# Optimization experiments

Measured on AMD Instinct MI355X. Metric: run time of the kernel, lower is better.

## Reference

```python
import jax, jax.numpy as jnp
import numpy as np

N_NODES = 50000
N_EDGES = 800000
IN_F = 128
OUT_F = 64


def setup_inputs() -> dict:
    key = jax.random.key(0)
    k1, k2, k3, k4, k5 = jax.random.split(key, 5)
    x = jax.random.normal(k1, (N_NODES, IN_F), dtype=jnp.float32)
    edge_index = jax.random.randint(k2, (2, N_EDGES), 0, N_NODES, dtype=jnp.int64)
    edge_weight = jax.random.uniform(k3, (N_EDGES,), dtype=jnp.float32)
    # Linear(in,out,bias=False): store as [in, out] so h = x @ W
    W = jax.random.normal(k4, (IN_F, OUT_F), dtype=jnp.float32) * (1.0 / np.sqrt(IN_F))
    # Linear(2*out, 1, bias=False): store as [2*out] vector
    a = jax.random.normal(k5, (2 * OUT_F,), dtype=jnp.float32) * (1.0 / np.sqrt(2 * OUT_F))
    return {"x": x, "edge_index": edge_index, "edge_weight": edge_weight, "W": W, "a": a}


def reference(x, edge_index, edge_weight, W, a):
    N = x.shape[0]
    F = W.shape[1]
    src, dst = edge_index[0], edge_index[1]
    h = x @ W  # [N, F]
    # a([h_src ; h_dst]) == h_src @ a[:F] + h_dst @ a[F:]  (no edge-level concat)
    s_src = h @ a[:F]   # [N]
    s_dst = h @ a[F:]   # [N]
    e = s_src[src] + s_dst[dst]            # [E]
    alpha = jax.nn.leaky_relu(e, negative_slope=0.2) * edge_weight
    alpha = alpha - jnp.max(alpha)         # global max subtraction, as in source
    alpha_exp = jnp.exp(alpha)             # [E]
    alpha_sum = jax.ops.segment_sum(alpha_exp, dst, num_segments=N)  # [N]
    alpha_norm = alpha_exp / (alpha_sum[dst] + 1e-8)                 # [E] (dropout = identity, eval mode)
    out = jax.ops.segment_sum(h[src] * alpha_norm[:, None], dst, num_segments=N)  # [N, F]
    return jax.nn.elu(out)
```

## Files before the change

kernel.cpp:

```cpp
#include <hip/hip_runtime.h>
#include <hip/hip_bf16.h>
#include <math.h>

#define FIN 128
#define FOUT 64
#define TM 64
#define XS_STRIDE 136

#define DB 64
#define CAP 1280
#define NBMAX 800
#define TILE_A 2048
#define EPT_A 8

typedef __attribute__((ext_vector_type(8))) short short8;
typedef __attribute__((ext_vector_type(4))) float floatx4;

static __device__ __forceinline__ unsigned short f2bf(float f) {
  __hip_bfloat16 b = __float2bfloat16(f);
  return *reinterpret_cast<unsigned short*>(&b);
}

__global__ __launch_bounds__(256) void k_gemm(
    const float* __restrict__ x, const float* __restrict__ W,
    const float* __restrict__ a, unsigned short* __restrict__ hbf,
    float* __restrict__ s_src, float* __restrict__ s_dst,
    int* __restrict__ bcur, int N)
{
  __shared__ unsigned short xsb[TM][XS_STRIDE];
  __shared__ unsigned short Wl[FOUT][XS_STRIDE];
  int t = threadIdx.x;
  int n0 = blockIdx.x * TM;

  int gid = blockIdx.x * 256 + t;
  if (gid < 800) bcur[gid] = 0;

  for (int i = t; i < FIN * FOUT; i += 256) {
    int k = i >> 6, f = i & 63;
    Wl[f][k] = f2bf(W[i]);
  }

#pragma unroll
  for (int i = 0; i < 8; i++) {
    int idx = t + i * 256;
    int row = idx >> 5, c4 = (idx & 31) * 4;
    int n = n0 + row;
    float4 v = make_float4(0.f, 0.f, 0.f, 0.f);
    if (n < N) v = *(const float4*)&x[(size_t)n * FIN + c4];
    ushort4 u = make_ushort4(f2bf(v.x), f2bf(v.y), f2bf(v.z), f2bf(v.w));
    *(ushort4*)&xsb[row][c4] = u;
  }
  __syncthreads();

  int lane = t & 63, w = t >> 6;
  int m = lane & 15, q = lane >> 4;

  short8 bf[4][4];
#pragma unroll
  for (int k0 = 0; k0 < 4; k0++)
#pragma unroll
    for (int j = 0; j < 4; j++)
      bf[k0][j] = *(const short8*)&Wl[j * 16 + m][k0 * 32 + q * 8];

  floatx4 acc[4];
#pragma unroll
  for (int j = 0; j < 4; j++) acc[j] = (floatx4){0.f, 0.f, 0.f, 0.f};

#pragma unroll
  for (int k0 = 0; k0 < 4; k0++) {
    short8 af = *(const short8*)&xsb[w * 16 + m][k0 * 32 + q * 8];
#pragma unroll
    for (int j = 0; j < 4; j++)
      acc[j] = __builtin_amdgcn_mfma_f32_16x16x32_bf16(af, bf[k0][j], acc[j], 0, 0, 0);
  }

  float av1[4], av2[4];
#pragma unroll
  for (int j = 0; j < 4; j++) {
    av1[j] = a[j * 16 + m];
    av2[j] = a[FOUT + j * 16 + m];
  }
  float s1r[4], s2r[4];
#pragma unroll
  for (int r = 0; r < 4; r++) {
    float c1 = 0.f, c2 = 0.f;
#pragma unroll
    for (int j = 0; j < 4; j++) {
      c1 = fmaf(acc[j][r], av1[j], c1);
      c2 = fmaf(acc[j][r], av2[j], c2);
    }
    s1r[r] = c1; s2r[r] = c2;
  }
#pragma unroll
  for (int o = 1; o < 16; o <<= 1) {
#pragma unroll
    for (int r = 0; r < 4; r++) {
      s1r[r] += __shfl_xor(s1r[r], o);
      s2r[r] += __shfl_xor(s2r[r], o);
    }
  }

#pragma unroll
  for (int j = 0; j < 4; j++)
#pragma unroll
    for (int r = 0; r < 4; r++) {
      int n = n0 + w * 16 + q * 4 + r;
      if (n < N) hbf[(size_t)n * FOUT + j * 16 + m] = f2bf(acc[j][r]);
    }
  if (m == 0) {
#pragma unroll
    for (int r = 0; r < 4; r++) {
      int n = n0 + w * 16 + q * 4 + r;
      if (n < N) { s_src[n] = s1r[r]; s_dst[n] = s2r[r]; }
    }
  }
}

__global__ __launch_bounds__(256) void k_bucketA(
    const int* __restrict__ src, const int* __restrict__ dst,
    const float* __restrict__ ew, const float* __restrict__ s_src,
    const float* __restrict__ s_dst, int* __restrict__ bcur,
    uint2* __restrict__ inter, int E, int nbuck)
{
  __shared__ uint2 stage[TILE_A];
  __shared__ int hist[NBMAX];
  __shared__ int sbase[NBMAX];
  __shared__ int gbase[NBMAX];
  __shared__ int wsum[4];

  int t = threadIdx.x;
  int base = blockIdx.x * TILE_A;
  int cntTile = E - base; if (cntTile > TILE_A) cntTile = TILE_A;

  for (int i = t; i < nbuck; i += 256) hist[i] = 0;
  __syncthreads();

  int sv[EPT_A], dv[EPT_A]; float evw[EPT_A]; int okm[EPT_A];
#pragma unroll
  for (int i = 0; i < EPT_A; i++) {
    int e = base + t + i * 256;
    okm[i] = (e < E);
    sv[i] = 0; dv[i] = 0; evw[i] = 0.f;
    if (okm[i]) { sv[i] = src[e]; dv[i] = dst[e]; evw[i] = ew[e]; }
  }

  float g1[EPT_A], g2[EPT_A];
#pragma unroll
  for (int i = 0; i < EPT_A; i++) {
    g1[i] = s_src[sv[i]];
    g2[i] = s_dst[dv[i]];
  }

  int lpos[EPT_A];
#pragma unroll
  for (int i = 0; i < EPT_A; i++)
    lpos[i] = okm[i] ? atomicAdd(&hist[dv[i] >> 6], 1) : -1;
  __syncthreads();

  int i0 = t * 4;
  int c0 = (i0 + 0 < nbuck) ? hist[i0 + 0] : 0;
  int c1 = (i0 + 1 < nbuck) ? hist[i0 + 1] : 0;
  int c2 = (i0 + 2 < nbuck) ? hist[i0 + 2] : 0;
  int c3 = (i0 + 3 < nbuck) ? hist[i0 + 3] : 0;
  int ts = c0 + c1 + c2 + c3;
  int lane = t & 63, wid = t >> 6;
  int inc = ts;
#pragma unroll
  for (int o = 1; o < 64; o <<= 1) {
    int up = __shfl_up(inc, o);
    if (lane >= o) inc += up;
  }
  if (lane == 63) wsum[wid] = inc;
  __syncthreads();
  int woff = 0;
  for (int w = 0; w < wid; w++) woff += wsum[w];
  int run = woff + inc - ts;
  if (i0 + 0 < nbuck) sbase[i0 + 0] = run; run += c0;
  if (i0 + 1 < nbuck) sbase[i0 + 1] = run; run += c1;
  if (i0 + 2 < nbuck) sbase[i0 + 2] = run; run += c2;
  if (i0 + 3 < nbuck) sbase[i0 + 3] = run;
  __syncthreads();

  for (int b = t; b < nbuck; b += 256)
    if (hist[b] > 0) gbase[b] = atomicAdd(&bcur[b], hist[b]);
  __syncthreads();

#pragma unroll
  for (int i = 0; i < EPT_A; i++) {
    if (lpos[i] >= 0) {
      float v = g1[i] + g2[i];
      v = (v > 0.f) ? v : 0.2f * v;
      v *= evw[i];
      unsigned key = ((unsigned)dv[i] << 16) | (unsigned)sv[i];
      stage[sbase[dv[i] >> 6] + lpos[i]] = make_uint2(key, __float_as_uint(__expf(v)));
    }
  }
  __syncthreads();

  for (int i = t; i < cntTile; i += 256) {
    uint2 en = stage[i];
    int b = en.x >> 22;
    int slot = gbase[b] + (i - sbase[b]);
    if (slot < CAP) inter[(size_t)b * CAP + slot] = en;
  }
}

__global__ __launch_bounds__(512) void k_bucketB(
    const uint2* __restrict__ inter, const int* __restrict__ bcur,
    const unsigned short* __restrict__ hbf, float* __restrict__ out, int N)
{
  __shared__ uint2 ss[CAP];
  __shared__ int hist[DB];
  __shared__ int rp[DB];
  int b = blockIdx.x;
  int t = threadIdx.x;
  int cnt = bcur[b]; if (cnt > CAP) cnt = CAP;

  if (t < DB) hist[t] = 0;
  __syncthreads();

  const uint2* bin = inter + (size_t)b * CAP;
  unsigned kx[3], ka[3]; int lp[3], dl[3];
#pragma unroll
  for (int i = 0; i < 3; i++) {
    int p = t + i * 512;
    lp[i] = -1;
    if (p < cnt) {
      uint2 en = bin[p];
      kx[i] = en.x; ka[i] = en.y;
      dl[i] = (en.x >> 16) & (DB - 1);
      lp[i] = atomicAdd(&hist[dl[i]], 1);
    }
  }
  __syncthreads();

  if (t < DB) {
    int v = hist[t];
    int inc = v;
#pragma unroll
    for (int o = 1; o < 64; o <<= 1) {
      int up = __shfl_up(inc, o);
      if (t >= o) inc += up;
    }
    rp[t] = inc - v;
  }
  __syncthreads();

#pragma unroll
  for (int i = 0; i < 3; i++)
    if (lp[i] >= 0) ss[rp[dl[i]] + lp[i]] = make_uint2(kx[i], ka[i]);
  __syncthreads();

  int grp = t >> 3, l = t & 7;
  int n = b * DB + grp;
  int beg = rp[grp];
  int end = beg + hist[grp];

  float acc[8];
#pragma unroll
  for (int i = 0; i < 8; i++) acc[i] = 0.f;
  float asum = 0.f;

  for (int p = beg; p < end; p += 4) {
    float aev[4]; uint4 rv[4];
#pragma unroll
    for (int u = 0; u < 4; u++) {
      aev[u] = 0.f;
      rv[u] = make_uint4(0u, 0u, 0u, 0u);
      if (p + u < end) {
        uint2 e = ss[p + u];
        aev[u] = __uint_as_float(e.y);
        rv[u] = ((const uint4*)(hbf + ((size_t)(e.x & 0xFFFFu) << 6)))[l];
      }
    }
#pragma unroll
    for (int u = 0; u < 4; u++) {
      asum += aev[u];
      const unsigned* uu = (const unsigned*)&rv[u];
#pragma unroll
      for (int i = 0; i < 4; i++) {
        float2 f = __bfloat1622float2(*(const __hip_bfloat162*)&uu[i]);
        acc[2 * i]     = fmaf(aev[u], f.x, acc[2 * i]);
        acc[2 * i + 1] = fmaf(aev[u], f.y, acc[2 * i + 1]);
      }
    }
  }

  if (n < N) {
    float inv = 1.f / (asum + 1e-8f);
    float v[8];
#pragma unroll
    for (int i = 0; i < 8; i++) {
      v[i] = acc[i] * inv;
      v[i] = (v[i] > 0.f) ? v[i] : expm1f(v[i]);
    }
    float* op = &out[(size_t)n * FOUT + l * 8];
    *(float4*)op       = make_float4(v[0], v[1], v[2], v[3]);
    *(float4*)(op + 4) = make_float4(v[4], v[5], v[6], v[7]);
  }
}

extern "C" void kernel_launch(void* const* d_in, const int* in_sizes, int n_in,
                              void* d_out, int out_size, void* d_ws, size_t ws_size,
                              hipStream_t stream)
{
  const float* x  = (const float*)d_in[0];
  const int*   ei = (const int*)d_in[1];
  const float* ew = (const float*)d_in[2];
  const float* W  = (const float*)d_in[3];
  const float* a  = (const float*)d_in[4];
  float* out = (float*)d_out;

  const int N = in_sizes[0] / FIN;
  const int E = in_sizes[2];
  const int* src = ei;
  const int* dst = ei + E;
  const int nbuck = (N + DB - 1) / DB;

  unsigned short* hbf = (unsigned short*)d_ws;
  float* ssrc  = (float*)(hbf + (size_t)N * FOUT);
  float* sdst  = ssrc + N;
  int*   bcur  = (int*)(sdst + N);
  uint2* inter = (uint2*)(bcur + 800);

  k_gemm<<<(N + TM - 1) / TM, 256, 0, stream>>>(x, W, a, hbf, ssrc, sdst, bcur, N);
  k_bucketA<<<(E + TILE_A - 1) / TILE_A, 256, 0, stream>>>(src, dst, ew, ssrc, sdst, bcur, inter, E, nbuck);
  k_bucketB<<<nbuck, 512, 0, stream>>>(inter, bcur, hbf, out, N);
}
```

Measured before the change: 124.7 us.

## Replace per-destination local sort with shared-memory atomic accumulation in bucket kernel

The aggregation kernel no longer counting-sorts each bucket's edges by destination in LDS before per-node accumulation. Each 8-thread group now takes edges directly and atomically adds weighted bf16-converted features into a padded shared accumulator and a denominator array. This removes the histogram, scan and scatter phases and their barriers and balances work across edges rather than nodes, but adds many LDS float atomics, which can contend when several edges hit the same destination.

```diff
diff --git a/kernel.cpp b/kernel.cpp
--- a/kernel.cpp
+++ b/kernel.cpp
@@ -12,6 +12,7 @@
 #define NBMAX 800
 #define TILE_A 2048
 #define EPT_A 8
+#define FPAD 66
 
 typedef __attribute__((ext_vector_type(8))) short short8;
 typedef __attribute__((ext_vector_type(4))) float floatx4;
@@ -209,90 +210,44 @@
     const uint2* __restrict__ inter, const int* __restrict__ bcur,
     const unsigned short* __restrict__ hbf, float* __restrict__ out, int N)
 {
-  __shared__ uint2 ss[CAP];
-  __shared__ int hist[DB];
-  __shared__ int rp[DB];
+  __shared__ float accf[DB][FPAD];
+  __shared__ float denom[DB];
   int b = blockIdx.x;
   int t = threadIdx.x;
   int cnt = bcur[b]; if (cnt > CAP) cnt = CAP;
 
-  if (t < DB) hist[t] = 0;
+  for (int i = t; i < DB * FPAD; i += 512) ((float*)accf)[i] = 0.f;
+  if (t < DB) denom[t] = 0.f;
   __syncthreads();
 
   const uint2* bin = inter + (size_t)b * CAP;
-  unsigned kx[3], ka[3]; int lp[3], dl[3];
-#pragma unroll
-  for (int i = 0; i < 3; i++) {
-    int p = t + i * 512;
-    lp[i] = -1;
-    if (p < cnt) {
-      uint2 en = bin[p];
-      kx[i] = en.x; ka[i] = en.y;
-      dl[i] = (en.x >> 16) & (DB - 1);
-      lp[i] = atomicAdd(&hist[dl[i]], 1);
-    }
-  }
-  __syncthreads();
-
-  if (t < DB) {
-    int v = hist[t];
-    int inc = v;
-#pragma unroll
-    for (int o = 1; o < 64; o <<= 1) {
-      int up = __shfl_up(inc, o);
-      if (t >= o) inc += up;
-    }
-    rp[t] = inc - v;
-  }
-  __syncthreads();
-
-#pragma unroll
-  for (int i = 0; i < 3; i++)
-    if (lp[i] >= 0) ss[rp[dl[i]] + lp[i]] = make_uint2(kx[i], ka[i]);
-  __syncthreads();
-
-  int grp = t >> 3, l = t & 7;
+  int eslot = t >> 3, l = t & 7;
+
+  for (int p = eslot; p < cnt; p += 64) {
+    uint2 e = bin[p];
+    int d = (e.x >> 16) & (DB - 1);
+    float ae = __uint_as_float(e.y);
+    uint4 r = ((const uint4*)(hbf + ((size_t)(e.x & 0xFFFFu) << 6)))[l];
+    if (l == 0) atomicAdd(&denom[d], ae);
+    const unsigned* u = (const unsigned*)&r;
+#pragma unroll
+    for (int i = 0; i < 4; i++) {
+      float2 f = __bfloat1622float2(*(const __hip_bfloat162*)&u[i]);
+      atomicAdd(&accf[d][l * 8 + 2 * i],     ae * f.x);
+      atomicAdd(&accf[d][l * 8 + 2 * i + 1], ae * f.y);
+    }
+  }
+  __syncthreads();
+
+  int grp = t >> 3;
   int n = b * DB + grp;
-  int beg = rp[grp];
-  int end = beg + hist[grp];
-
-  float acc[8];
-#pragma unroll
-  for (int i = 0; i < 8; i++) acc[i] = 0.f;
-  float asum = 0.f;
-
-  for (int p = beg; p < end; p += 4) {
-    float aev[4]; uint4 rv[4];
-#pragma unroll
-    for (int u = 0; u < 4; u++) {
-      aev[u] = 0.f;
-      rv[u] = make_uint4(0u, 0u, 0u, 0u);
-      if (p + u < end) {
-        uint2 e = ss[p + u];
-        aev[u] = __uint_as_float(e.y);
-        rv[u] = ((const uint4*)(hbf + ((size_t)(e.x & 0xFFFFu) << 6)))[l];
-      }
-    }
-#pragma unroll
-    for (int u = 0; u < 4; u++) {
-      asum += aev[u];
-      const unsigned* uu = (const unsigned*)&rv[u];
-#pragma unroll
-      for (int i = 0; i < 4; i++) {
-        float2 f = __bfloat1622float2(*(const __hip_bfloat162*)&uu[i]);
-        acc[2 * i]     = fmaf(aev[u], f.x, acc[2 * i]);
-        acc[2 * i + 1] = fmaf(aev[u], f.y, acc[2 * i + 1]);
-      }
-    }
-  }
-
   if (n < N) {
-    float inv = 1.f / (asum + 1e-8f);
+    float inv = 1.f / (denom[grp] + 1e-8f);
     float v[8];
 #pragma unroll
     for (int i = 0; i < 8; i++) {
-      v[i] = acc[i] * inv;
-      v[i] = (v[i] > 0.f) ? v[i] : expm1f(v[i]);
+      float x = accf[grp][l * 8 + i] * inv;
+      v[i] = (x > 0.f) ? x : expm1f(x);
     }
     float* op = &out[(size_t)n * FOUT + l * 8];
     *(float4*)op       = make_float4(v[0], v[1], v[2], v[3]);
```

After: 455.3 us. 3.65x slower.
